# Optimization experiments

Hardware: AMD Instinct MI355X
Metric: run time of the kernel (lower is better)

Reference implementation:

```python
import jax, jax.numpy as jnp
import numpy as np

SCORE_THR = 0.5
RADII = jnp.array([0.5, 0.6, 0.7], dtype=jnp.float32)  # radius_dict[c]; all labels 0..C-1 covered

B, N, C = 2, 8192, 3


def setup_inputs() -> dict:
    key = jax.random.key(0)
    k1, k2 = jax.random.split(key)
    xyz = jax.random.normal(k1, (B, N, 3), dtype=jnp.float32)
    cls_features = jax.random.normal(k2, (B, N, C), dtype=jnp.float32)
    return {"xyz": xyz, "cls_features": cls_features}


def _greedy_select(xyz, cls_features):
    """Greedy per-class radius suppression over the flattened batch.
    Returns sample_idx (B, L) int32, zero-padded exactly like the torch code
    (sample_idx is zeros except slot i of the batch owning selection i)."""
    b, n, _ = xyz.shape
    L = b * n
    scores = jax.nn.sigmoid(jnp.max(cls_features, axis=2))   # (B, N)
    labels = jnp.argmax(cls_features, axis=2)                # (B, N)
    valid = scores >= SCORE_THR

    flat_scores = jnp.where(valid, scores, -jnp.inf).reshape(L)
    order = jnp.argsort(-flat_scores)                        # descending score; invalid sink to end
    sorted_labels = labels.reshape(L)[order]
    sorted_valid = valid.reshape(L)[order]
    sorted_batch = (order // n).astype(jnp.int32)
    sorted_pts = xyz.reshape(L, 3)[order]

    def cond(state):
        i, remaining, _ = state
        return remaining.any() & (i < L)

    def body(state):
        i, remaining, sel_pos = state
        cur = jnp.argmax(remaining)                  # first remaining point in sorted order
        # NB: faithful to the original bug: radius chosen via sorted_labels[i]
        # (loop counter), not the label of the current point.
        r = RADII[sorted_labels[i]]
        d2 = jnp.sum((sorted_pts - sorted_pts[cur]) ** 2, axis=-1)  # (L,)
        suppress = (sorted_batch == sorted_batch[cur]) & (d2 <= r * r)
        return (i + 1, remaining & ~suppress, sel_pos.at[i].set(cur.astype(jnp.int32)))

    sel0 = jnp.full((L,), -1, dtype=jnp.int32)
    _, _, sel_pos = jax.lax.while_loop(cond, body, (jnp.int32(0), sorted_valid, sel0))

    picked = sel_pos >= 0
    orig = jnp.where(picked, order[jnp.maximum(sel_pos, 0)], 0)  # flat index in [0, L)
    bidx = jnp.where(picked, orig // n, 0)
    pidx = jnp.where(picked, orig % n, 0)
    slots = jnp.arange(L)
    # zeros init + scatter exactly mirrors torch: sample_idx[batch, i] = point
    sample_idx = jnp.zeros((b, L), dtype=jnp.int32).at[bidx, slots].set(pidx.astype(jnp.int32))
    return sample_idx


def reference(xyz, cls_features):
    sample_idx = _greedy_select(xyz, cls_features)
    bsz = xyz.shape[0]
    # gather_operation: new_xyz[b, m] = xyz[b, sample_idx[b, m]]
    new_xyz = xyz[jnp.arange(bsz)[:, None], sample_idx]          # (B, L, 3)
    return new_xyz, sample_idx
```

## Files before the change

### kernel.cpp

```cpp
#include <hip/hip_runtime.h>
#include <stdint.h>


#define L_TOT 16384
#define NPT   8192

__device__ __forceinline__ int cellco(float v) {
    int c = (int)floorf((v + 6.4f) * 1.25f);
    return c < 0 ? 0 : (c > 15 ? 15 : c);
}
__device__ __forceinline__ float d2f(float ax, float ay, float az,
                                     float bx, float by, float bz) {
    float dx = __fsub_rn(ax, bx), dy = __fsub_rn(ay, by), dz = __fsub_rn(az, bz);
    return __fadd_rn(__fadd_rn(__fmul_rn(dx, dx), __fmul_rn(dy, dy)), __fmul_rn(dz, dz));
}
__device__ __forceinline__ float rad2(int lb) {
    float rr = (lb == 0) ? 0.5f : ((lb == 1) ? 0.6f : 0.7f);
    return __fmul_rn(rr, rr);
}
__device__ __forceinline__ float rlf(float v, int l) {
    return __uint_as_float(__builtin_amdgcn_readlane(__float_as_uint(v), l));
}
__device__ __forceinline__ int rli(int v, int l) {
    return (int)__builtin_amdgcn_readlane((uint32_t)v, l);
}

__global__ void k1_keys(const float* __restrict__ cls, uint64_t* __restrict__ keys,
                        uint8_t* __restrict__ umeta, uint16_t* __restrict__ sample,
                        int* __restrict__ cellcnt) {
    int l = blockIdx.x * blockDim.x + threadIdx.x;
    if (l >= L_TOT) return;
    ((uint32_t*)sample)[l] = 0;
    if (l < 8192) cellcnt[l] = 0;
    float c0 = cls[l * 3 + 0], c1 = cls[l * 3 + 1], c2 = cls[l * 3 + 2];
    float m = c0; int lab = 0;
    if (c1 > m) { m = c1; lab = 1; }
    if (c2 > m) { m = c2; lab = 2; }
    int valid = (m >= 0.0f) ? 1 : 0;
    float keyf = valid ? m : -__builtin_inff();
    uint32_t u = __float_as_uint(keyf);
    uint32_t o = (u & 0x80000000u) ? ~u : (u | 0x80000000u);
    keys[l] = ((uint64_t)(~o) << 32) | (uint32_t)l;
    umeta[l] = (uint8_t)(lab | (valid << 2));
}

__global__ void __launch_bounds__(256) k2_sort(
    const uint64_t* __restrict__ keys, const uint8_t* __restrict__ umeta,
    const float* __restrict__ xyz,
    float4* __restrict__ spts, uint8_t* __restrict__ slab, uint16_t* __restrict__ sorder,
    int* __restrict__ cellcnt) {
    __shared__ uint64_t tile[2048];
    __shared__ int psum[256];
    const int t = threadIdx.x;
    const int elem = t & 31, part = t >> 5;
    const int l = blockIdx.x * 32 + elem;
    const uint64_t myk = keys[l];
    int cnt = 0;
    for (int t0 = 0; t0 < L_TOT; t0 += 2048) {
        for (int j = t; j < 2048; j += 256) tile[j] = keys[t0 + j];
        __syncthreads();
        const int b0 = part * 256;
        #pragma unroll 4
        for (int j = 0; j < 256; ++j) cnt += (tile[b0 + j] < myk) ? 1 : 0;
        __syncthreads();
    }
    psum[t] = cnt;
    __syncthreads();
    if (t < 32) {
        int rank = 0;
        #pragma unroll
        for (int q = 0; q < 8; ++q) rank += psum[q * 32 + t];
        const int ll = blockIdx.x * 32 + t;
        int b = ll >> 13, p = ll & (NPT - 1);
        const float* src = xyz + ((size_t)(b * NPT + p)) * 3;
        float x = src[0], y = src[1], z = src[2];
        uint8_t mt = umeta[ll];
        int lab = mt & 3, valid = (mt >> 2) & 1;
        float4 v; v.x = x; v.y = y; v.z = z;
        v.w = __uint_as_float((uint32_t)(b | (valid << 1)));
        spts[rank] = v;
        slab[rank] = (uint8_t)lab;
        sorder[rank] = (uint16_t)ll;
        if (valid) {
            int cl = (b << 12) | (cellco(z) << 8) | (cellco(y) << 4) | cellco(x);
            atomicAdd(&cellcnt[cl], 1);
        }
    }
}

__global__ void g2_scan(int* __restrict__ cellcnt, int* __restrict__ cellstart) {
    __shared__ int part[256];
    __shared__ int poff[256];
    int t = threadIdx.x;
    int base = t * 32;
    int loc[32];
    int s = 0;
    for (int k = 0; k < 32; ++k) { loc[k] = cellcnt[base + k]; s += loc[k]; }
    part[t] = s;
    __syncthreads();
    if (t == 0) {
        int run = 0;
        for (int q = 0; q < 256; ++q) { poff[q] = run; run += part[q]; }
    }
    __syncthreads();
    int run = poff[t];
    for (int k = 0; k < 32; ++k) {
        cellstart[base + k] = run; run += loc[k];
        cellcnt[base + k] = 0;
    }
    if (t == 255) cellstart[8192] = run;
}

__global__ void g3_scatter(const float4* __restrict__ spts, const int* __restrict__ cellstart,
                           int* __restrict__ cellfill, float4* __restrict__ cellxyz) {
    int pos = blockIdx.x * blockDim.x + threadIdx.x;
    if (pos >= L_TOT) return;
    float4 v = spts[pos];
    uint32_t w = __float_as_uint(v.w);
    if (!(w & 2u)) return;
    int b = (int)(w & 1u);
    int cl = (b << 12) | (cellco(v.z) << 8) | (cellco(v.y) << 4) | cellco(v.x);
    int slot = atomicAdd(&cellfill[cl], 1);
    float4 o; o.x = v.x; o.y = v.y; o.z = v.z; o.w = __uint_as_float((uint32_t)pos);
    cellxyz[cellstart[cl] + slot] = o;
}

__global__ void __launch_bounds__(1024) k3_greedy(
    const float4* __restrict__ spts, const uint8_t* __restrict__ slab,
    const uint16_t* __restrict__ sorder,
    const int* __restrict__ cellstart, const float4* __restrict__ cellxyz,
    uint16_t* __restrict__ sample) {
    __shared__ uint32_t rem[512];
    __shared__ uint16_t cs16[8193];
    __shared__ uint8_t  slds[L_TOT];
    __shared__ float4   pkd[2][128];
    __shared__ int      pkb[2][128];
    __shared__ int      pkn[2];

    const int t = threadIdx.x;
    const int V = cellstart[8192];
    const int NPH = (V + 127) >> 7;

    float4 cv0 = make_float4(0,0,0,0), cv1 = make_float4(0,0,0,0);
    int cord0 = 0, cord1 = 0;
    if (t < 64) {
        cv0 = spts[t]; cv1 = spts[64 + t];
        cord0 = (int)sorder[t]; cord1 = (int)sorder[64 + t];
    }
    for (int j = t; j < 8193; j += 1024) cs16[j] = (uint16_t)cellstart[j];
    for (int j = t; j < L_TOT; j += 1024) slds[j] = slab[j];
    for (int w = t; w < 512; w += 1024) {
        int lo = w * 32;
        uint32_t m;
        if (V >= lo + 32) m = 0xFFFFFFFFu;
        else if (V <= lo) m = 0u;
        else m = (1u << (V - lo)) - 1u;
        rem[w] = m;
    }
    if (t < 2) pkn[t] = 0;
    __syncthreads();

    int ii = 0;
    for (int ph = 0; ph < NPH; ++ph) {
        const int cur = ph & 1, prv = cur ^ 1;
        if (t < 64) {
            const int nb = (ph + 1) << 7;
            int q0 = nb + t;       q0 = q0 > (L_TOT - 1) ? (L_TOT - 1) : q0;
            int q1 = nb + 64 + t;  q1 = q1 > (L_TOT - 1) ? (L_TOT - 1) : q1;
            float4 nv0 = spts[q0], nv1 = spts[q1];
            int nord0 = (int)sorder[q0], nord1 = (int)sorder[q1];

            int o0 = ii + t;      o0 = o0 > (L_TOT - 1) ? (L_TOT - 1) : o0;
            int o1 = ii + 64 + t; o1 = o1 > (L_TOT - 1) ? (L_TOT - 1) : o1;
            float cr0 = rad2((int)slds[o0]);
            float cr1 = rad2((int)slds[o1]);

            const int pos0 = (ph << 7) + t, pos1 = pos0 + 64;
            bool a0 = (pos0 < V) && ((rem[pos0 >> 5] >> (pos0 & 31)) & 1u);
            bool a1 = (pos1 < V) && ((rem[pos1 >> 5] >> (pos1 & 31)) & 1u);
            const int cb0 = cord0 >> 13, cb1 = cord1 >> 13;
            const int m = pkn[prv];
            for (int j = 0; j < m; ++j) {
                float4 pk = pkd[prv][j];
                int pb = pkb[prv][j];
                if (a0 && cb0 == pb &&
                    d2f(cv0.x, cv0.y, cv0.z, pk.x, pk.y, pk.z) <= pk.w) a0 = false;
                if (a1 && cb1 == pb &&
                    d2f(cv1.x, cv1.y, cv1.z, pk.x, pk.y, pk.z) <= pk.w) a1 = false;
            }

            int np = 0;
            const int ii0 = ii;
            {
                unsigned long long am = __ballot(a0 ? 1 : 0);
                while (am) {
                    const int jl0 = (int)__builtin_ctzll(am);
                    const unsigned long long am2 = am & (am - 1);
                    const bool has2 = (am2 != 0ull);
                    const int jl1 = has2 ? (int)__builtin_ctzll(am2) : jl0;
                    const float p0x = rlf(cv0.x, jl0), p0y = rlf(cv0.y, jl0), p0z = rlf(cv0.z, jl0);
                    const int   b0  = rli(cord0, jl0) >> 13;
                    const float p1x = rlf(cv0.x, jl1), p1y = rlf(cv0.y, jl1), p1z = rlf(cv0.z, jl1);
                    const int   b1  = rli(cord0, jl1) >> 13;
                    const float r2_0 = rlf((np & 64) ? cr1 : cr0, np & 63);
                    const int np1 = np + 1;
                    const float r2_1 = rlf((np1 & 64) ? cr1 : cr0, np1 & 63);
                    const bool kb = (b0 == b1) &&
                                    (d2f(p1x, p1y, p1z, p0x, p0y, p0z) <= r2_0);
                    const bool two = has2 && !kb;
                    if (t == jl0) {
                        pkd[cur][np] = make_float4(cv0.x, cv0.y, cv0.z, r2_0);
                        pkb[cur][np] = b0;
                        sample[b0 * L_TOT + ii0 + np] = (uint16_t)(cord0 & (NPT - 1));
                    }
                    if (two && t == jl1) {
                        pkd[cur][np1] = make_float4(cv0.x, cv0.y, cv0.z, r2_1);
                        pkb[cur][np1] = b1;
                        sample[b1 * L_TOT + ii0 + np1] = (uint16_t)(cord0 & (NPT - 1));
                    }
                    if (a0) {
                        if (cb0 == b0 && d2f(cv0.x, cv0.y, cv0.z, p0x, p0y, p0z) <= r2_0) a0 = false;
                        if (two && cb0 == b1 && d2f(cv0.x, cv0.y, cv0.z, p1x, p1y, p1z) <= r2_1) a0 = false;
                    }
                    if (a1) {
                        if (cb1 == b0 && d2f(cv1.x, cv1.y, cv1.z, p0x, p0y, p0z) <= r2_0) a1 = false;
                        if (two && cb1 == b1 && d2f(cv1.x, cv1.y, cv1.z, p1x, p1y, p1z) <= r2_1) a1 = false;
                    }
                    np += two ? 2 : 1;
                    am = __ballot(a0 ? 1 : 0);
                }
            }
            {
                unsigned long long am = __ballot(a1 ? 1 : 0);
                while (am) {
                    const int jl0 = (int)__builtin_ctzll(am);
                    const unsigned long long am2 = am & (am - 1);
                    const bool has2 = (am2 != 0ull);
                    const int jl1 = has2 ? (int)__builtin_ctzll(am2) : jl0;
                    const float p0x = rlf(cv1.x, jl0), p0y = rlf(cv1.y, jl0), p0z = rlf(cv1.z, jl0);
                    const int   b0  = rli(cord1, jl0) >> 13;
                    const float p1x = rlf(cv1.x, jl1), p1y = rlf(cv1.y, jl1), p1z = rlf(cv1.z, jl1);
                    const int   b1  = rli(cord1, jl1) >> 13;
                    const float r2_0 = rlf((np & 64) ? cr1 : cr0, np & 63);
                    const int np1 = np + 1;
                    const float r2_1 = rlf((np1 & 64) ? cr1 : cr0, np1 & 63);
                    const bool kb = (b0 == b1) &&
                                    (d2f(p1x, p1y, p1z, p0x, p0y, p0z) <= r2_0);
                    const bool two = has2 && !kb;
                    if (t == jl0) {
                        pkd[cur][np] = make_float4(cv1.x, cv1.y, cv1.z, r2_0);
                        pkb[cur][np] = b0;
                        sample[b0 * L_TOT + ii0 + np] = (uint16_t)(cord1 & (NPT - 1));
                    }
                    if (two && t == jl1) {
                        pkd[cur][np1] = make_float4(cv1.x, cv1.y, cv1.z, r2_1);
                        pkb[cur][np1] = b1;
                        sample[b1 * L_TOT + ii0 + np1] = (uint16_t)(cord1 & (NPT - 1));
                    }
                    if (a1) {
                        if (cb1 == b0 && d2f(cv1.x, cv1.y, cv1.z, p0x, p0y, p0z) <= r2_0) a1 = false;
                        if (two && cb1 == b1 && d2f(cv1.x, cv1.y, cv1.z, p1x, p1y, p1z) <= r2_1) a1 = false;
                    }
                    np += two ? 2 : 1;
                    am = __ballot(a1 ? 1 : 0);
                }
            }
            ii = ii0 + np;
            if (t == 0) pkn[cur] = np;
            cv0 = nv0; cv1 = nv1; cord0 = nord0; cord1 = nord1;
        } else {
            const int np = pkn[prv];
            if (np > 0) {
                const int tid = t - 64;
                const int ntask = np * 216;
                for (int task = tid; task < ntask; task += 960) {
                    int sub = task & 7;
                    int pc = task >> 3;
                    int p = pc / 27;
                    int c = pc - p * 27;
                    float4 pv = pkd[prv][p];
                    int pb_ = pkb[prv][p];
                    float r2 = pv.w;
                    int cx = cellco(pv.x) + (c % 3) - 1;
                    int cy = cellco(pv.y) + ((c / 3) % 3) - 1;
                    int cz = cellco(pv.z) + (c / 9) - 1;
                    if ((unsigned)cx > 15u || (unsigned)cy > 15u || (unsigned)cz > 15u) continue;
                    float lox = -6.4f + 0.8f * cx, hix = lox + 0.8f;
                    float loy = -6.4f + 0.8f * cy, hiy = loy + 0.8f;
                    float loz = -6.4f + 0.8f * cz, hiz = loz + 0.8f;
                    if (cx == 0) lox = -1e30f;  if (cx == 15) hix = 1e30f;
                    if (cy == 0) loy = -1e30f;  if (cy == 15) hiy = 1e30f;
                    if (cz == 0) loz = -1e30f;  if (cz == 15) hiz = 1e30f;
                    float dx = fmaxf(fmaxf(lox - pv.x, pv.x - hix), 0.0f);
                    float dy = fmaxf(fmaxf(loy - pv.y, pv.y - hiy), 0.0f);
                    float dz = fmaxf(fmaxf(loz - pv.z, pv.z - hiz), 0.0f);
                    if (dx * dx + dy * dy + dz * dz > r2 + 0.02f) continue;
                    int cl = (pb_ << 12) | (cz << 8) | (cy << 4) | cx;
                    int st = (int)cs16[cl];
                    int en = (int)cs16[cl + 1];
                    for (int k = st + sub; k < en; k += 8) {
                        float4 q = cellxyz[k];
                        float d2 = d2f(q.x, q.y, q.z, pv.x, pv.y, pv.z);
                        if (d2 <= r2) {
                            uint32_t qp = __float_as_uint(q.w);
                            atomicAnd(&rem[qp >> 5], ~(1u << (qp & 31)));
                        }
                    }
                }
            }
        }
        __syncthreads();
    }
}

__global__ void k4_out(const float* __restrict__ xyz, const uint16_t* __restrict__ sample,
                       float* __restrict__ out) {
    int s = blockIdx.x * blockDim.x + threadIdx.x;
    if (s >= 2 * L_TOT) return;
    int idx = (int)sample[s];
    int b = s >> 14;
    const float* src = xyz + ((size_t)(b * NPT + idx)) * 3;
    float* dst = out + (size_t)s * 3;
    dst[0] = src[0]; dst[1] = src[1]; dst[2] = src[2];
    out[3 * 2 * L_TOT + s] = (float)idx;
}

extern "C" void kernel_launch(void* const* d_in, const int* in_sizes, int n_in,
                              void* d_out, int out_size, void* d_ws, size_t ws_size,
                              hipStream_t stream) {
    const float* xyz = (const float*)d_in[0];
    const float* cls = (const float*)d_in[1];
    float* out = (float*)d_out;
    char* ws = (char*)d_ws;
    float4*   spts    = (float4*)  (ws + 0);
    uint8_t*  slab    = (uint8_t*) (ws + 262144);
    uint16_t* sorder  = (uint16_t*)(ws + 278528);
    int*      cellcnt = (int*)     (ws + 311296);
    int*      cellst  = (int*)     (ws + 344064);
    float4*   cellxyz = (float4*)  (ws + 380928);
    uint64_t* keys    = (uint64_t*)(ws + 380928);
    uint8_t*  umeta   = (uint8_t*) (ws + 512000);
    uint16_t* sample  = (uint16_t*)(ws + 643072);

    k1_keys   <<<64,  256, 0, stream>>>(cls, keys, umeta, sample, cellcnt);
    k2_sort   <<<512, 256, 0, stream>>>(keys, umeta, xyz, spts, slab, sorder, cellcnt);
    g2_scan   <<<1,   256, 0, stream>>>(cellcnt, cellst);
    g3_scatter<<<64,  256, 0, stream>>>(spts, cellst, cellcnt, cellxyz);
    k3_greedy <<<1,  1024, 0, stream>>>(spts, slab, sorder, cellst, cellxyz, sample);
    k4_out    <<<128, 256, 0, stream>>>(xyz, sample, out);
}
```

Measured before the change: 616.2 us.

## Stage quantized cell points in LDS and pack labels to 2 bits

The greedy kernel now preloads every valid point as a 64-bit quantized packed entry into shared memory (128KB). The suppression loop tests distance on these fixed-point coordinates and falls back to an exact global float check only inside an uncertainty band. It also keeps a per-cell-slot alive bitmask so points already suppressed are skipped, and packs labels as 2-bit fields so the label table fits in LDS. A wave-level ballot skips the pending-pick check when no lanes are active. This cuts global memory traffic in the serial greedy kernel, at the cost of a large LDS footprint and added quantization bookkeeping.

New measurement: 508.7 us. 1.21x faster.

```diff
diff --git a/kernel.cpp b/kernel.cpp
--- a/kernel.cpp
+++ b/kernel.cpp
@@ -27,11 +27,12 @@
 
 __global__ void k1_keys(const float* __restrict__ cls, uint64_t* __restrict__ keys,
                         uint8_t* __restrict__ umeta, uint16_t* __restrict__ sample,
-                        int* __restrict__ cellcnt) {
+                        int* __restrict__ cellcnt, uint32_t* __restrict__ slab2) {
     int l = blockIdx.x * blockDim.x + threadIdx.x;
     if (l >= L_TOT) return;
     ((uint32_t*)sample)[l] = 0;
     if (l < 8192) cellcnt[l] = 0;
+    if (l < 1024) slab2[l] = 0;
     float c0 = cls[l * 3 + 0], c1 = cls[l * 3 + 1], c2 = cls[l * 3 + 2];
     float m = c0; int lab = 0;
     if (c1 > m) { m = c1; lab = 1; }
@@ -47,7 +48,7 @@
 __global__ void __launch_bounds__(256) k2_sort(
     const uint64_t* __restrict__ keys, const uint8_t* __restrict__ umeta,
     const float* __restrict__ xyz,
-    float4* __restrict__ spts, uint8_t* __restrict__ slab, uint16_t* __restrict__ sorder,
+    float4* __restrict__ spts, uint32_t* __restrict__ slab2, uint16_t* __restrict__ sorder,
     int* __restrict__ cellcnt) {
     __shared__ uint64_t tile[2048];
     __shared__ int psum[256];
@@ -79,8 +80,8 @@
         float4 v; v.x = x; v.y = y; v.z = z;
         v.w = __uint_as_float((uint32_t)(b | (valid << 1)));
         spts[rank] = v;
-        slab[rank] = (uint8_t)lab;
         sorder[rank] = (uint16_t)ll;
+        atomicOr(&slab2[rank >> 4], (uint32_t)lab << ((rank & 15) << 1));
         if (valid) {
             int cl = (b << 12) | (cellco(z) << 8) | (cellco(y) << 4) | cellco(x);
             atomicAdd(&cellcnt[cl], 1);
@@ -126,13 +127,15 @@
 }
 
 __global__ void __launch_bounds__(1024) k3_greedy(
-    const float4* __restrict__ spts, const uint8_t* __restrict__ slab,
+    const float4* __restrict__ spts, const uint32_t* __restrict__ slab2,
     const uint16_t* __restrict__ sorder,
     const int* __restrict__ cellstart, const float4* __restrict__ cellxyz,
     uint16_t* __restrict__ sample) {
+    __shared__ uint64_t qpack[16384];
     __shared__ uint32_t rem[512];
-    __shared__ uint16_t cs16[8193];
-    __shared__ uint8_t  slds[L_TOT];
+    __shared__ uint32_t alive2[512];
+    __shared__ uint16_t cs16[8194];
+    __shared__ uint32_t slds2[1024];
     __shared__ float4   pkd[2][128];
     __shared__ int      pkb[2][128];
     __shared__ int      pkn[2];
@@ -148,7 +151,19 @@
         cord0 = (int)sorder[t]; cord1 = (int)sorder[64 + t];
     }
     for (int j = t; j < 8193; j += 1024) cs16[j] = (uint16_t)cellstart[j];
-    for (int j = t; j < L_TOT; j += 1024) slds[j] = slab[j];
+    for (int j = t; j < 1024; j += 1024) slds2[j] = slab2[j];
+    for (int k = t; k < V; k += 1024) {
+        float4 q = cellxyz[k];
+        int qx = __float2int_rn(__fmul_rn(__fadd_rn(q.x, 8.0f), 4096.0f));
+        int qy = __float2int_rn(__fmul_rn(__fadd_rn(q.y, 8.0f), 4096.0f));
+        int qz = __float2int_rn(__fmul_rn(__fadd_rn(q.z, 8.0f), 4096.0f));
+        qx = qx < 0 ? 0 : (qx > 65535 ? 65535 : qx);
+        qy = qy < 0 ? 0 : (qy > 65535 ? 65535 : qy);
+        qz = qz < 0 ? 0 : (qz > 65535 ? 65535 : qz);
+        uint32_t pos = __float_as_uint(q.w);
+        qpack[k] = ((uint64_t)(((uint32_t)qz) | (pos << 16)) << 32)
+                 | ((uint32_t)qx | ((uint32_t)qy << 16));
+    }
     for (int w = t; w < 512; w += 1024) {
         int lo = w * 32;
         uint32_t m;
@@ -156,6 +171,7 @@
         else if (V <= lo) m = 0u;
         else m = (1u << (V - lo)) - 1u;
         rem[w] = m;
+        alive2[w] = m;
     }
     if (t < 2) pkn[t] = 0;
     __syncthreads();
@@ -172,21 +188,23 @@
 
             int o0 = ii + t;      o0 = o0 > (L_TOT - 1) ? (L_TOT - 1) : o0;
             int o1 = ii + 64 + t; o1 = o1 > (L_TOT - 1) ? (L_TOT - 1) : o1;
-            float cr0 = rad2((int)slds[o0]);
-            float cr1 = rad2((int)slds[o1]);
+            float cr0 = rad2((int)((slds2[o0 >> 4] >> ((o0 & 15) << 1)) & 3u));
+            float cr1 = rad2((int)((slds2[o1 >> 4] >> ((o1 & 15) << 1)) & 3u));
 
             const int pos0 = (ph << 7) + t, pos1 = pos0 + 64;
             bool a0 = (pos0 < V) && ((rem[pos0 >> 5] >> (pos0 & 31)) & 1u);
             bool a1 = (pos1 < V) && ((rem[pos1 >> 5] >> (pos1 & 31)) & 1u);
             const int cb0 = cord0 >> 13, cb1 = cord1 >> 13;
-            const int m = pkn[prv];
-            for (int j = 0; j < m; ++j) {
-                float4 pk = pkd[prv][j];
-                int pb = pkb[prv][j];
-                if (a0 && cb0 == pb &&
-                    d2f(cv0.x, cv0.y, cv0.z, pk.x, pk.y, pk.z) <= pk.w) a0 = false;
-                if (a1 && cb1 == pb &&
-                    d2f(cv1.x, cv1.y, cv1.z, pk.x, pk.y, pk.z) <= pk.w) a1 = false;
+            if (__ballot((a0 ? 1 : 0) | (a1 ? 1 : 0))) {
+                const int m = pkn[prv];
+                for (int j = 0; j < m; ++j) {
+                    float4 pk = pkd[prv][j];
+                    int pb = pkb[prv][j];
+                    if (a0 && cb0 == pb &&
+                        d2f(cv0.x, cv0.y, cv0.z, pk.x, pk.y, pk.z) <= pk.w) a0 = false;
+                    if (a1 && cb1 == pb &&
+                        d2f(cv1.x, cv1.y, cv1.z, pk.x, pk.y, pk.z) <= pk.w) a1 = false;
+                }
             }
 
             int np = 0;
@@ -291,19 +309,38 @@
                     if (cx == 0) lox = -1e30f;  if (cx == 15) hix = 1e30f;
                     if (cy == 0) loy = -1e30f;  if (cy == 15) hiy = 1e30f;
                     if (cz == 0) loz = -1e30f;  if (cz == 15) hiz = 1e30f;
-                    float dx = fmaxf(fmaxf(lox - pv.x, pv.x - hix), 0.0f);
-                    float dy = fmaxf(fmaxf(loy - pv.y, pv.y - hiy), 0.0f);
-                    float dz = fmaxf(fmaxf(loz - pv.z, pv.z - hiz), 0.0f);
-                    if (dx * dx + dy * dy + dz * dz > r2 + 0.02f) continue;
+                    float bdx = fmaxf(fmaxf(lox - pv.x, pv.x - hix), 0.0f);
+                    float bdy = fmaxf(fmaxf(loy - pv.y, pv.y - hiy), 0.0f);
+                    float bdz = fmaxf(fmaxf(loz - pv.z, pv.z - hiz), 0.0f);
+                    if (bdx * bdx + bdy * bdy + bdz * bdz > r2 + 0.02f) continue;
                     int cl = (pb_ << 12) | (cz << 8) | (cy << 4) | cx;
                     int st = (int)cs16[cl];
                     int en = (int)cs16[cl + 1];
+                    float psx = (pv.x + 8.0f) * 4096.0f;
+                    float psy = (pv.y + 8.0f) * 4096.0f;
+                    float psz = (pv.z + 8.0f) * 4096.0f;
+                    float thr_hi = (r2 + 0.02f) * 16777216.0f;
+                    float thr_lo = (r2 - 0.02f) * 16777216.0f;
                     for (int k = st + sub; k < en; k += 8) {
-                        float4 q = cellxyz[k];
-                        float d2 = d2f(q.x, q.y, q.z, pv.x, pv.y, pv.z);
-                        if (d2 <= r2) {
-                            uint32_t qp = __float_as_uint(q.w);
-                            atomicAnd(&rem[qp >> 5], ~(1u << (qp & 31)));
+                        uint64_t e = qpack[k];
+                        uint32_t lo = (uint32_t)e, hi = (uint32_t)(e >> 32);
+                        float ddx = (float)(lo & 0xffffu) - psx;
+                        float ddy = (float)(lo >> 16) - psy;
+                        float ddz = (float)(hi & 0xffffu) - psz;
+                        float d2s = ddx * ddx + ddy * ddy + ddz * ddz;
+                        if (d2s <= thr_hi) {
+                            if (alive2[k >> 5] & (1u << (k & 31))) {
+                                bool sup = (d2s <= thr_lo);
+                                if (!sup) {
+                                    float4 q = cellxyz[k];
+                                    sup = d2f(q.x, q.y, q.z, pv.x, pv.y, pv.z) <= r2;
+                                }
+                                if (sup) {
+                                    uint32_t pos = hi >> 16;
+                                    atomicAnd(&alive2[k >> 5], ~(1u << (k & 31)));
+                                    atomicAnd(&rem[pos >> 5], ~(1u << (pos & 31)));
+                                }
+                            }
                         }
                     }
                 }
@@ -333,7 +370,7 @@
     float* out = (float*)d_out;
     char* ws = (char*)d_ws;
     float4*   spts    = (float4*)  (ws + 0);
-    uint8_t*  slab    = (uint8_t*) (ws + 262144);
+    uint32_t* slab2   = (uint32_t*)(ws + 262144);
     uint16_t* sorder  = (uint16_t*)(ws + 278528);
     int*      cellcnt = (int*)     (ws + 311296);
     int*      cellst  = (int*)     (ws + 344064);
@@ -342,10 +379,10 @@
     uint8_t*  umeta   = (uint8_t*) (ws + 512000);
     uint16_t* sample  = (uint16_t*)(ws + 643072);
 
-    k1_keys   <<<64,  256, 0, stream>>>(cls, keys, umeta, sample, cellcnt);
-    k2_sort   <<<512, 256, 0, stream>>>(keys, umeta, xyz, spts, slab, sorder, cellcnt);
+    k1_keys   <<<64,  256, 0, stream>>>(cls, keys, umeta, sample, cellcnt, slab2);
+    k2_sort   <<<512, 256, 0, stream>>>(keys, umeta, xyz, spts, slab2, sorder, cellcnt);
     g2_scan   <<<1,   256, 0, stream>>>(cellcnt, cellst);
     g3_scatter<<<64,  256, 0, stream>>>(spts, cellst, cellcnt, cellxyz);
-    k3_greedy <<<1,  1024, 0, stream>>>(spts, slab, sorder, cellst, cellxyz, sample);
+    k3_greedy <<<1,  1024, 0, stream>>>(spts, slab2, sorder, cellst, cellxyz, sample);
     k4_out    <<<128, 256, 0, stream>>>(xyz, sample, out);
 }
```
